# Optimization experiments

Measured on AMD Instinct MI355X. Metric: run time of the kernel, lower is better.

## Reference

```python
import jax, jax.numpy as jnp
import numpy as np

N_HEAD = 16


def setup_inputs() -> dict:
    key = jax.random.key(0)
    ks = jax.random.split(key, 4)
    B, S, E = 1, 4096, 1024
    x = jax.random.normal(ks[0], (B, S, E), dtype=jnp.float32)
    # causal mask: True where attention is DISALLOWED (upper triangle)
    masked_matrix = ~jnp.tril(jnp.ones((S, S), dtype=bool))[None, None]
    Wqkv = jax.random.normal(ks[1], (E, 3 * E), dtype=jnp.float32) * (1.0 / np.sqrt(E))
    bqkv = jnp.zeros((3 * E,), dtype=jnp.float32)
    Wp = jax.random.normal(ks[2], (E, E), dtype=jnp.float32) * (1.0 / np.sqrt(E))
    bp = jnp.zeros((E,), dtype=jnp.float32)
    return {"x": x, "masked_matrix": masked_matrix, "Wqkv": Wqkv, "bqkv": bqkv,
            "Wp": Wp, "bp": bp}


def reference(x, masked_matrix, Wqkv, bqkv, Wp, bp):
    B, S, E = x.shape
    H = N_HEAD
    D = E // H
    qkv = x @ Wqkv + bqkv                        # [B,S,3E]
    q, k, v = jnp.split(qkv, 3, axis=-1)
    q = q.reshape(B, S, H, D).transpose(0, 2, 1, 3)  # [B,H,S,D]
    k = k.reshape(B, S, H, D).transpose(0, 2, 1, 3)
    v = v.reshape(B, S, H, D).transpose(0, 2, 1, 3)
    # NOTE: source applies NO 1/sqrt(D) scaling — kept faithful.
    att = jnp.einsum('bhqd,bhkd->bhqk', q, k)    # [B,H,S,S]
    att = jnp.where(masked_matrix, jnp.float32(-jnp.inf), att)
    att = jax.nn.softmax(att, axis=-1)
    res = jnp.einsum('bhqk,bhkd->bhqd', att, v)  # [B,H,S,D]
    res = res.transpose(0, 2, 1, 3).reshape(B, S, E)
    return res @ Wp + bp
```

## Files before the change

### kernel.cpp

```cpp
#include <hip/hip_runtime.h>
#include <hip/hip_bf16.h>
#include <math.h>

#define S_LEN 4096
#define EMB   1024
#define NHEAD 16
#define HDIM  64

typedef __attribute__((ext_vector_type(8))) _Float16 half8;
typedef __attribute__((ext_vector_type(4))) _Float16 half4;
typedef __attribute__((ext_vector_type(4))) float float4_t;
typedef __attribute__((ext_vector_type(16))) float float16_t;
typedef __attribute__((ext_vector_type(4))) int int4_t;
typedef __attribute__((ext_vector_type(2))) int int2_t;

#define GLOBAL_AS(p) ((const __attribute__((address_space(1))) void*)(p))
#define LDS_AS(p)    ((__attribute__((address_space(3))) void*)(p))

#define LOG2E 1.4426950408889634f

__global__ __launch_bounds__(256) void prep(
    const float* __restrict__ x, const float* __restrict__ Wqkv,
    const float* __restrict__ Wp,
    _Float16* __restrict__ xh, _Float16* __restrict__ WTh,
    _Float16* __restrict__ WpT)
{
    const int bid = blockIdx.x;
    if (bid < 4096) {
        const int i = bid * 256 + threadIdx.x;
        const float4_t v = ((const float4_t*)x)[i];
        half4 hh;
#pragma unroll
        for (int j = 0; j < 4; ++j) hh[j] = (_Float16)v[j];
        ((half4*)xh)[i] = hh;
        return;
    }
    __shared__ float t[64][65];
    const float* in;
    _Float16* out;
    int R, C, bx, by;
    if (bid < 4096 + 768) {
        const int idx = bid - 4096;
        bx = idx % 48; by = idx / 48;
        in = Wqkv; out = WTh; R = 1024; C = 3072;
    } else {
        const int idx = bid - 4864;
        bx = idx & 15; by = idx >> 4;
        in = Wp; out = WpT; R = 1024; C = 1024;
    }
    const int r0 = by * 64, c0 = bx * 64;
    for (int i = threadIdx.x; i < 64 * 64; i += 256) {
        int r = i >> 6, c = i & 63;
        t[r][c] = in[(size_t)(r0 + r) * C + c0 + c];
    }
    __syncthreads();
    for (int i = threadIdx.x; i < 64 * 64; i += 256) {
        int c = i >> 6, r = i & 63;
        out[(size_t)(c0 + c) * R + r0 + r] = (_Float16)t[r][c];
    }
}

__global__ __launch_bounds__(256) void gemm_qkv(
    const _Float16* __restrict__ Ag, const _Float16* __restrict__ Bg,
    const float* __restrict__ bias,
    _Float16* __restrict__ qk, _Float16* __restrict__ vt, int K)
{
    constexpr int BK = 32;
    __shared__ _Float16 Ah[128 * BK];
    __shared__ _Float16 Bh[128 * BK];

    const int tid = threadIdx.x;
    const int wave = tid >> 6, lane = tid & 63;
    const int l16 = lane & 15, quad = lane >> 4;
    const int wr = wave >> 1, wc = wave & 1;
    const int row0 = blockIdx.y * 128, col0 = blockIdx.x * 128;
    const int lrow = lane >> 2, lc8 = (lane & 3) * 8;

    float4_t acc[4][4];
#pragma unroll
    for (int i = 0; i < 4; ++i)
#pragma unroll
        for (int j = 0; j < 4; ++j) acc[i][j] = (float4_t){0.f, 0.f, 0.f, 0.f};

    for (int k0 = 0; k0 < K; k0 += BK) {
        __syncthreads();
#pragma unroll
        for (int i = 0; i < 2; ++i) {
            const int ar = i * 64 + wave * 16;
            __builtin_amdgcn_global_load_lds(
                GLOBAL_AS(Ag + (size_t)(row0 + ar + lrow) * K + k0 + lc8),
                LDS_AS(&Ah[ar * BK]), 16, 0, 0);
            __builtin_amdgcn_global_load_lds(
                GLOBAL_AS(Bg + (size_t)(col0 + ar + lrow) * K + k0 + lc8),
                LDS_AS(&Bh[ar * BK]), 16, 0, 0);
        }
        __syncthreads();

        half8 af[4], bfr[4];
#pragma unroll
        for (int t = 0; t < 4; ++t) {
            af[t]  = *(const half8*)&Ah[(wr * 64 + t * 16 + l16) * BK + quad * 8];
            bfr[t] = *(const half8*)&Bh[(wc * 64 + t * 16 + l16) * BK + quad * 8];
        }
#pragma unroll
        for (int i = 0; i < 4; ++i)
#pragma unroll
            for (int j = 0; j < 4; ++j)
                acc[i][j] = __builtin_amdgcn_mfma_f32_16x16x32_f16(af[i], bfr[j], acc[i][j], 0, 0, 0);
    }

#pragma unroll
    for (int i = 0; i < 4; ++i) {
#pragma unroll
        for (int j = 0; j < 4; ++j) {
            const int colb = col0 + wc * 64 + j * 16 + l16;
            const float bv = bias[colb];
            const int rowb = row0 + wr * 64 + i * 16 + quad * 4;
            if (colb < 2048) {
                const float sc = (colb >= 1024) ? LOG2E : 1.0f;
#pragma unroll
                for (int r = 0; r < 4; ++r)
                    qk[(size_t)(rowb + r) * 2048 + colb] =
                        (_Float16)((acc[i][j][r] + bv) * sc);
            } else {
                half4 w;
#pragma unroll
                for (int r = 0; r < 4; ++r) w[r] = (_Float16)(acc[i][j][r] + bv);
                *(half4*)&vt[(size_t)(colb - 2048) * 4096 + rowb] = w;
            }
        }
    }
}

__global__ __launch_bounds__(256) void gemm_out(
    const _Float16* __restrict__ Ag, const _Float16* __restrict__ Bg,
    const float* __restrict__ bias, float* __restrict__ C, int N, int K)
{
    constexpr int BK = 32;
    __shared__ _Float16 Ah[128 * BK];
    __shared__ _Float16 Bh[64 * BK];

    const int tid = threadIdx.x;
    const int wave = tid >> 6, lane = tid & 63;
    const int l16 = lane & 15, quad = lane >> 4;
    const int row0 = blockIdx.y * 128, col0 = blockIdx.x * 64;
    const int lrow = lane >> 2, lc8 = (lane & 3) * 8;

    float4_t acc[2][4];
#pragma unroll
    for (int i = 0; i < 2; ++i)
#pragma unroll
        for (int j = 0; j < 4; ++j) acc[i][j] = (float4_t){0.f, 0.f, 0.f, 0.f};

    for (int k0 = 0; k0 < K; k0 += BK) {
        __syncthreads();
#pragma unroll
        for (int i = 0; i < 2; ++i) {
            const int ar = i * 64 + wave * 16;
            __builtin_amdgcn_global_load_lds(
                GLOBAL_AS(Ag + (size_t)(row0 + ar + lrow) * K + k0 + lc8),
                LDS_AS(&Ah[ar * BK]), 16, 0, 0);
        }
        {
            const int br = wave * 16;
            __builtin_amdgcn_global_load_lds(
                GLOBAL_AS(Bg + (size_t)(col0 + br + lrow) * K + k0 + lc8),
                LDS_AS(&Bh[br * BK]), 16, 0, 0);
        }
        __syncthreads();

        half8 af[2], bfr[4];
#pragma unroll
        for (int t = 0; t < 2; ++t)
            af[t] = *(const half8*)&Ah[(wave * 32 + t * 16 + l16) * BK + quad * 8];
#pragma unroll
        for (int t = 0; t < 4; ++t)
            bfr[t] = *(const half8*)&Bh[(t * 16 + l16) * BK + quad * 8];
#pragma unroll
        for (int i = 0; i < 2; ++i)
#pragma unroll
            for (int j = 0; j < 4; ++j)
                acc[i][j] = __builtin_amdgcn_mfma_f32_16x16x32_f16(af[i], bfr[j], acc[i][j], 0, 0, 0);
    }

#pragma unroll
    for (int i = 0; i < 2; ++i) {
#pragma unroll
        for (int j = 0; j < 4; ++j) {
            const int colb = col0 + j * 16 + l16;
            const float bv = bias[colb];
#pragma unroll
            for (int r = 0; r < 4; ++r) {
                const int row = row0 + wave * 32 + i * 16 + quad * 4 + r;
                C[(size_t)row * N + colb] = acc[i][j][r] + bv;
            }
        }
    }
}

__global__ __launch_bounds__(256, 4) void flash_attn_f16(
    const _Float16* __restrict__ qk, const _Float16* __restrict__ v_t,
    _Float16* __restrict__ opart, float* __restrict__ mlpart)
{
    __shared__ __align__(16) _Float16 KsT[2][64 * 64];
    __shared__ __align__(16) _Float16 VtT[2][64 * 64];

    const int bid  = blockIdx.x;
    const int g    = bid & 255;
    const int hv   = g & 15;
    const int h    = (hv & 7) * 2 + (hv >> 3);
    const int j    = g >> 4;
    const int v    = bid >> 8;
    const int tile = (v & 1) ? (31 - j) : j;
    const int split= v >> 1;

    const int wave = threadIdx.x >> 6;
    const int lane = threadIdx.x & 63;
    const int l31  = lane & 31;
    const int hi   = lane >> 5;

    const int dma_r = wave * 16 + (lane >> 3);
    const int dma_c = ((lane & 7) ^ (lane >> 3)) * 8;

    const _Float16* kplane = qk + 1024 + h * HDIM;
    const _Float16* vplane = v_t + (size_t)h * HDIM * 4096;

    const int q0 = tile * 128 + wave * 32;

    half8 qf[4];
#pragma unroll
    for (int jj = 0; jj < 4; ++jj)
        qf[jj] = *(const half8*)(qk + (size_t)(q0 + l31) * 2048 + h * HDIM
                                 + jj * 16 + hi * 8);

    float16_t o0 = (float16_t)0.f, o1 = (float16_t)0.f;
    float m_r = -INFINITY, l_r = 0.f;

    const int kb0 = 64 * split;
#pragma unroll
    for (int p = 0; p < 2; ++p) {
        const int r = dma_r + p * 8;
        __builtin_amdgcn_global_load_lds(
            GLOBAL_AS(kplane + (size_t)(kb0 + r) * 2048 + dma_c),
            LDS_AS(&KsT[0][(wave * 128 + p * 64) * 8]), 16, 0, 0);
        __builtin_amdgcn_global_load_lds(
            GLOBAL_AS(vplane + (size_t)r * 4096 + kb0 + dma_c),
            LDS_AS(&VtT[0][(wave * 128 + p * 64) * 8]), 16, 0, 0);
    }

    int ib = 0;
    int kb = kb0;
    for (int it = 0; it <= tile; ++it, kb += 128, ib ^= 1) {
        __syncthreads();

        if (it < tile) {
            const int kn = kb + 128;
#pragma unroll
            for (int p = 0; p < 2; ++p) {
                const int r = dma_r + p * 8;
                __builtin_amdgcn_global_load_lds(
                    GLOBAL_AS(kplane + (size_t)(kn + r) * 2048 + dma_c),
                    LDS_AS(&KsT[ib ^ 1][(wave * 128 + p * 64) * 8]), 16, 0, 0);
                __builtin_amdgcn_global_load_lds(
                    GLOBAL_AS(vplane + (size_t)r * 4096 + kn + dma_c),
                    LDS_AS(&VtT[ib ^ 1][(wave * 128 + p * 64) * 8]), 16, 0, 0);
            }
        }

        if (kb <= q0 + 31) {
            float16_t s0 = (float16_t)0.f, s1 = (float16_t)0.f;
            __builtin_amdgcn_s_setprio(1);
#pragma unroll
            for (int jj = 0; jj < 4; ++jj) {
                const int r7 = l31 & 7;
                const half8 kf0 = *(const half8*)&KsT[ib][
                    ((l31) * 8 + ((2 * jj + hi) ^ r7)) * 8];
                const half8 kf1 = *(const half8*)&KsT[ib][
                    ((32 + l31) * 8 + ((2 * jj + hi) ^ r7)) * 8];
                s0 = __builtin_amdgcn_mfma_f32_32x32x16_f16(kf0, qf[jj], s0, 0, 0, 0);
                s1 = __builtin_amdgcn_mfma_f32_32x32x16_f16(kf1, qf[jj], s1, 0, 0, 0);
            }
            __builtin_amdgcn_s_setprio(0);

            if (kb + 63 > q0) {
                const int qg = q0 + l31;
#pragma unroll
                for (int gg = 0; gg < 4; ++gg)
#pragma unroll
                    for (int r = 0; r < 4; ++r) {
                        const int keyb = kb + r + 8 * gg + 4 * hi;
                        if (keyb > qg)      s0[4 * gg + r] = -INFINITY;
                        if (keyb + 32 > qg) s1[4 * gg + r] = -INFINITY;
                    }
            }

            float mx = s0[0];
#pragma unroll
            for (int i = 1; i < 16; ++i) mx = fmaxf(mx, s0[i]);
#pragma unroll
            for (int i = 0; i < 16; ++i) mx = fmaxf(mx, s1[i]);
            mx = fmaxf(mx, __shfl_xor(mx, 32));
            const bool  grow  = mx > m_r + 8.0f;
            const float mnew  = grow ? mx : m_r;
            const float alpha = __builtin_amdgcn_exp2f(m_r - mnew);

            int w0[8], w1[8];
            float lsum = 0.f;
#pragma unroll
            for (int i = 0; i < 8; ++i) {
                const float pa = __builtin_amdgcn_exp2f(s0[2 * i]     - mnew);
                const float pb = __builtin_amdgcn_exp2f(s0[2 * i + 1] - mnew);
                lsum += pa + pb;
                w0[i] = __builtin_bit_cast(int, __builtin_amdgcn_cvt_pkrtz(pa, pb));
            }
#pragma unroll
            for (int i = 0; i < 8; ++i) {
                const float pa = __builtin_amdgcn_exp2f(s1[2 * i]     - mnew);
                const float pb = __builtin_amdgcn_exp2f(s1[2 * i + 1] - mnew);
                lsum += pa + pb;
                w1[i] = __builtin_bit_cast(int, __builtin_amdgcn_cvt_pkrtz(pa, pb));
            }
            l_r = l_r * alpha + lsum;
            m_r = mnew;
            if (__any(grow)) {
#pragma unroll
                for (int i = 0; i < 16; ++i) { o0[i] *= alpha; o1[i] *= alpha; }
            }

            half8 pf[4];
            {
                const int2_t a02 = __builtin_amdgcn_permlane32_swap(w0[0], w0[2], 0, 0);
                const int2_t a13 = __builtin_amdgcn_permlane32_swap(w0[1], w0[3], 0, 0);
                const int2_t a46 = __builtin_amdgcn_permlane32_swap(w0[4], w0[6], 0, 0);
                const int2_t a57 = __builtin_amdgcn_permlane32_swap(w0[5], w0[7], 0, 0);
                int4_t f0 = {a02[0], a13[0], a02[1], a13[1]};
                int4_t f1 = {a46[0], a57[0], a46[1], a57[1]};
                pf[0] = __builtin_bit_cast(half8, f0);
                pf[1] = __builtin_bit_cast(half8, f1);
                const int2_t b02 = __builtin_amdgcn_permlane32_swap(w1[0], w1[2], 0, 0);
                const int2_t b13 = __builtin_amdgcn_permlane32_swap(w1[1], w1[3], 0, 0);
                const int2_t b46 = __builtin_amdgcn_permlane32_swap(w1[4], w1[6], 0, 0);
                const int2_t b57 = __builtin_amdgcn_permlane32_swap(w1[5], w1[7], 0, 0);
                int4_t f2 = {b02[0], b13[0], b02[1], b13[1]};
                int4_t f3 = {b46[0], b57[0], b46[1], b57[1]};
                pf[2] = __builtin_bit_cast(half8, f2);
                pf[3] = __builtin_bit_cast(half8, f3);
            }

            __builtin_amdgcn_s_setprio(1);
#pragma unroll
            for (int kc = 0; kc < 4; ++kc) {
                const int r7 = l31 & 7;
                const half8 vf0 = *(const half8*)&VtT[ib][
                    ((l31) * 8 + ((2 * kc + hi) ^ r7)) * 8];
                const half8 vf1 = *(const half8*)&VtT[ib][
                    ((32 + l31) * 8 + ((2 * kc + hi) ^ r7)) * 8];
                o0 = __builtin_amdgcn_mfma_f32_32x32x16_f16(vf0, pf[kc], o0, 0, 0, 0);
                o1 = __builtin_amdgcn_mfma_f32_32x32x16_f16(vf1, pf[kc], o1, 0, 0, 0);
            }
            __builtin_amdgcn_s_setprio(0);
        }
    }

    const float lr = l_r + __shfl_xor(l_r, 32);
    const size_t prow = (size_t)(split * 4096 + q0 + l31);
#pragma unroll
    for (int gg = 0; gg < 4; ++gg) {
        half4 wa, wb;
#pragma unroll
        for (int r = 0; r < 4; ++r) {
            wa[r] = (_Float16)o0[4 * gg + r];
            wb[r] = (_Float16)o1[4 * gg + r];
        }
        const size_t base = prow * 1024 + h * HDIM + 8 * gg + 4 * hi;
        *(half4*)&opart[base]      = wa;
        *(half4*)&opart[base + 32] = wb;
    }
    if (hi == 0) {
        float2 ml; ml.x = m_r; ml.y = lr;
        ((float2*)mlpart)[prow * 16 + h] = ml;
    }
}

__global__ __launch_bounds__(256) void combine(
    const _Float16* __restrict__ opart, const float* __restrict__ mlpart,
    _Float16* __restrict__ resh)
{
    const int idx = blockIdx.x * 256 + threadIdx.x;
    const int row = idx >> 7;
    const int c8  = (idx & 127) * 8;
    const int h   = c8 >> 6;
    const float2 ml0 = ((const float2*)mlpart)[(size_t)row * 16 + h];
    const float2 ml1 = ((const float2*)mlpart)[(size_t)(4096 + row) * 16 + h];
    const float m  = fmaxf(ml0.x, ml1.x);
    const float a0 = __builtin_amdgcn_exp2f(ml0.x - m);
    const float a1 = __builtin_amdgcn_exp2f(ml1.x - m);
    const float inv = 1.0f / (ml0.y * a0 + ml1.y * a1);
    const half8 o0 = *(const half8*)&opart[(size_t)row * 1024 + c8];
    const half8 o1 = *(const half8*)&opart[(size_t)(4096 + row) * 1024 + c8];
    half8 w;
#pragma unroll
    for (int jj = 0; jj < 8; ++jj)
        w[jj] = (_Float16)(((float)o0[jj] * a0 + (float)o1[jj] * a1) * inv);
    *(half8*)&resh[(size_t)row * 1024 + c8] = w;
}

extern "C" void kernel_launch(void* const* d_in, const int* in_sizes, int n_in,
                              void* d_out, int out_size, void* d_ws, size_t ws_size,
                              hipStream_t stream)
{
    const float* x    = (const float*)d_in[0];
    const float* Wqkv = (const float*)d_in[2];
    const float* bqkv = (const float*)d_in[3];
    const float* Wp   = (const float*)d_in[4];
    const float* bp   = (const float*)d_in[5];
    float* out = (float*)d_out;

    _Float16* xh  = (_Float16*)d_ws;
    _Float16* WTh = xh + (size_t)4096 * 1024;
    _Float16* qkh = WTh + (size_t)3072 * 1024;
    _Float16* vtg = qkh + (size_t)4096 * 2048;
    _Float16* WpT = vtg + (size_t)1024 * 4096;
    _Float16* opart = WpT + (size_t)1024 * 1024;
    float* mlpart = (float*)(opart + (size_t)2 * 4096 * 1024);
    _Float16* resh = xh;

    dim3 blk(256);

    prep<<<dim3(5120), blk, 0, stream>>>(x, Wqkv, Wp, xh, WTh, WpT);

    gemm_qkv<<<dim3(3072 / 128, 4096 / 128), blk, 0, stream>>>(
        xh, WTh, bqkv, qkh, vtg, 1024);

    flash_attn_f16<<<dim3(1024), dim3(256), 0, stream>>>(qkh, vtg, opart, mlpart);

    combine<<<dim3(2048), blk, 0, stream>>>(opart, mlpart, resh);

    gemm_out<<<dim3(1024 / 64, 4096 / 128), blk, 0, stream>>>(
        resh, WpT, bp, out, 1024, 1024);
}
```

Measured before the change: 245.6 us.

## Stage QKV epilogue through LDS, swizzle GEMM block order, tree-reduce softmax max

Result: no change. 244.3 us (-0.5%).

```diff
diff --git a/kernel.cpp b/kernel.cpp
--- a/kernel.cpp
+++ b/kernel.cpp
@@ -68,12 +68,15 @@
     constexpr int BK = 32;
     __shared__ _Float16 Ah[128 * BK];
     __shared__ _Float16 Bh[128 * BK];
+    __shared__ __align__(16) _Float16 Tq[128][136];
 
     const int tid = threadIdx.x;
     const int wave = tid >> 6, lane = tid & 63;
     const int l16 = lane & 15, quad = lane >> 4;
     const int wr = wave >> 1, wc = wave & 1;
-    const int row0 = blockIdx.y * 128, col0 = blockIdx.x * 128;
+    const int lid = blockIdx.y * 24 + blockIdx.x;
+    const int swz = (lid & 7) * 96 + (lid >> 3);
+    const int row0 = (swz / 24) * 128, col0 = (swz % 24) * 128;
     const int lrow = lane >> 2, lc8 = (lane & 3) * 8;
 
     float4_t acc[4][4];
@@ -109,25 +112,42 @@
                 acc[i][j] = __builtin_amdgcn_mfma_f32_16x16x32_f16(af[i], bfr[j], acc[i][j], 0, 0, 0);
     }
 
+    const bool  isV = (col0 >= 2048);
+    const float sc  = (col0 >= 1024 && col0 < 2048) ? LOG2E : 1.0f;
 #pragma unroll
     for (int i = 0; i < 4; ++i) {
 #pragma unroll
         for (int j = 0; j < 4; ++j) {
-            const int colb = col0 + wc * 64 + j * 16 + l16;
-            const float bv = bias[colb];
-            const int rowb = row0 + wr * 64 + i * 16 + quad * 4;
-            if (colb < 2048) {
-                const float sc = (colb >= 1024) ? LOG2E : 1.0f;
+            const int col = wc * 64 + j * 16 + l16;
+            const float bv = bias[col0 + col];
+            const int row = wr * 64 + i * 16 + quad * 4;
+            if (isV) {
 #pragma unroll
                 for (int r = 0; r < 4; ++r)
-                    qk[(size_t)(rowb + r) * 2048 + colb] =
-                        (_Float16)((acc[i][j][r] + bv) * sc);
+                    Tq[col][row + r] = (_Float16)(acc[i][j][r] + bv);
             } else {
-                half4 w;
-#pragma unroll
-                for (int r = 0; r < 4; ++r) w[r] = (_Float16)(acc[i][j][r] + bv);
-                *(half4*)&vt[(size_t)(colb - 2048) * 4096 + rowb] = w;
-            }
+#pragma unroll
+                for (int r = 0; r < 4; ++r)
+                    Tq[row + r][col] = (_Float16)((acc[i][j][r] + bv) * sc);
+            }
+        }
+    }
+    __syncthreads();
+    if (isV) {
+        _Float16* base = vt + (size_t)(col0 - 2048) * 4096 + row0;
+#pragma unroll
+        for (int pass = 0; pass < 8; ++pass) {
+            const int c  = pass * 16 + (tid >> 4);
+            const int ch = (tid & 15) * 8;
+            *(half8*)&base[(size_t)c * 4096 + ch] = *(const half8*)&Tq[c][ch];
+        }
+    } else {
+        _Float16* base = qk + (size_t)row0 * 2048 + col0;
+#pragma unroll
+        for (int pass = 0; pass < 8; ++pass) {
+            const int r  = pass * 16 + (tid >> 4);
+            const int ch = (tid & 15) * 8;
+            *(half8*)&base[(size_t)r * 2048 + ch] = *(const half8*)&Tq[r][ch];
         }
     }
 }
@@ -143,7 +163,9 @@
     const int tid = threadIdx.x;
     const int wave = tid >> 6, lane = tid & 63;
     const int l16 = lane & 15, quad = lane >> 4;
-    const int row0 = blockIdx.y * 128, col0 = blockIdx.x * 64;
+    const int lid = blockIdx.y * 16 + blockIdx.x;
+    const int swz = (lid & 7) * 64 + (lid >> 3);
+    const int row0 = (swz / 16) * 128, col0 = (swz % 16) * 64;
     const int lrow = lane >> 2, lc8 = (lane & 3) * 8;
 
     float4_t acc[2][4];
@@ -294,32 +316,43 @@
                     }
             }
 
-            float mx = s0[0];
-#pragma unroll
-            for (int i = 1; i < 16; ++i) mx = fmaxf(mx, s0[i]);
-#pragma unroll
-            for (int i = 0; i < 16; ++i) mx = fmaxf(mx, s1[i]);
+            float a0 = fmaxf(s0[0], s0[1]),  a1 = fmaxf(s0[2], s0[3]);
+            float a2 = fmaxf(s0[4], s0[5]),  a3 = fmaxf(s0[6], s0[7]);
+            float a4 = fmaxf(s0[8], s0[9]),  a5 = fmaxf(s0[10], s0[11]);
+            float a6 = fmaxf(s0[12], s0[13]), a7 = fmaxf(s0[14], s0[15]);
+            float b0 = fmaxf(s1[0], s1[1]),  b1 = fmaxf(s1[2], s1[3]);
+            float b2 = fmaxf(s1[4], s1[5]),  b3 = fmaxf(s1[6], s1[7]);
+            float b4 = fmaxf(s1[8], s1[9]),  b5 = fmaxf(s1[10], s1[11]);
+            float b6 = fmaxf(s1[12], s1[13]), b7 = fmaxf(s1[14], s1[15]);
+            a0 = fmaxf(a0, a1); a2 = fmaxf(a2, a3);
+            a4 = fmaxf(a4, a5); a6 = fmaxf(a6, a7);
+            b0 = fmaxf(b0, b1); b2 = fmaxf(b2, b3);
+            b4 = fmaxf(b4, b5); b6 = fmaxf(b6, b7);
+            a0 = fmaxf(a0, a2); a4 = fmaxf(a4, a6);
+            b0 = fmaxf(b0, b2); b4 = fmaxf(b4, b6);
+            float mx = fmaxf(fmaxf(a0, a4), fmaxf(b0, b4));
             mx = fmaxf(mx, __shfl_xor(mx, 32));
             const bool  grow  = mx > m_r + 8.0f;
             const float mnew  = grow ? mx : m_r;
             const float alpha = __builtin_amdgcn_exp2f(m_r - mnew);
 
             int w0[8], w1[8];
-            float lsum = 0.f;
+            float ls0 = 0.f, ls1 = 0.f, ls2 = 0.f, ls3 = 0.f;
 #pragma unroll
             for (int i = 0; i < 8; ++i) {
                 const float pa = __builtin_amdgcn_exp2f(s0[2 * i]     - mnew);
                 const float pb = __builtin_amdgcn_exp2f(s0[2 * i + 1] - mnew);
-                lsum += pa + pb;
+                if (i & 1) ls1 += pa + pb; else ls0 += pa + pb;
                 w0[i] = __builtin_bit_cast(int, __builtin_amdgcn_cvt_pkrtz(pa, pb));
             }
 #pragma unroll
             for (int i = 0; i < 8; ++i) {
                 const float pa = __builtin_amdgcn_exp2f(s1[2 * i]     - mnew);
                 const float pb = __builtin_amdgcn_exp2f(s1[2 * i + 1] - mnew);
-                lsum += pa + pb;
+                if (i & 1) ls3 += pa + pb; else ls2 += pa + pb;
                 w1[i] = __builtin_bit_cast(int, __builtin_amdgcn_cvt_pkrtz(pa, pb));
             }
+            const float lsum = (ls0 + ls1) + (ls2 + ls3);
             l_r = l_r * alpha + lsum;
             m_r = mnew;
             if (__any(grow)) {
@@ -329,20 +362,20 @@
 
             half8 pf[4];
             {
-                const int2_t a02 = __builtin_amdgcn_permlane32_swap(w0[0], w0[2], 0, 0);
-                const int2_t a13 = __builtin_amdgcn_permlane32_swap(w0[1], w0[3], 0, 0);
-                const int2_t a46 = __builtin_amdgcn_permlane32_swap(w0[4], w0[6], 0, 0);
-                const int2_t a57 = __builtin_amdgcn_permlane32_swap(w0[5], w0[7], 0, 0);
-                int4_t f0 = {a02[0], a13[0], a02[1], a13[1]};
-                int4_t f1 = {a46[0], a57[0], a46[1], a57[1]};
+                const int2_t c02 = __builtin_amdgcn_permlane32_swap(w0[0], w0[2], 0, 0);
+                const int2_t c13 = __builtin_amdgcn_permlane32_swap(w0[1], w0[3], 0, 0);
+                const int2_t c46 = __builtin_amdgcn_permlane32_swap(w0[4], w0[6], 0, 0);
+                const int2_t c57 = __builtin_amdgcn_permlane32_swap(w0[5], w0[7], 0, 0);
+                int4_t f0 = {c02[0], c13[0], c02[1], c13[1]};
+                int4_t f1 = {c46[0], c57[0], c46[1], c57[1]};
                 pf[0] = __builtin_bit_cast(half8, f0);
                 pf[1] = __builtin_bit_cast(half8, f1);
-                const int2_t b02 = __builtin_amdgcn_permlane32_swap(w1[0], w1[2], 0, 0);
-                const int2_t b13 = __builtin_amdgcn_permlane32_swap(w1[1], w1[3], 0, 0);
-                const int2_t b46 = __builtin_amdgcn_permlane32_swap(w1[4], w1[6], 0, 0);
-                const int2_t b57 = __builtin_amdgcn_permlane32_swap(w1[5], w1[7], 0, 0);
-                int4_t f2 = {b02[0], b13[0], b02[1], b13[1]};
-                int4_t f3 = {b46[0], b57[0], b46[1], b57[1]};
+                const int2_t d02 = __builtin_amdgcn_permlane32_swap(w1[0], w1[2], 0, 0);
+                const int2_t d13 = __builtin_amdgcn_permlane32_swap(w1[1], w1[3], 0, 0);
+                const int2_t d46 = __builtin_amdgcn_permlane32_swap(w1[4], w1[6], 0, 0);
+                const int2_t d57 = __builtin_amdgcn_permlane32_swap(w1[5], w1[7], 0, 0);
+                int4_t f2 = {d02[0], d13[0], d02[1], d13[1]};
+                int4_t f3 = {d46[0], d57[0], d46[1], d57[1]};
                 pf[2] = __builtin_bit_cast(half8, f2);
                 pf[3] = __builtin_bit_cast(half8, f3);
             }
```
